# Kernel tuning notes

Measured on AMD Instinct MI355X. Metric: run time of the kernel, lower is better.

The kernel has to match this reference:

```python
import jax, jax.numpy as jnp
import numpy as np

N = 100000
D = 128      # embedding_dim
HID = 32     # hidden per head
HEADS = 4
OUT_C = 64
E = 1600000
NEG_SLOPE = 0.2


def setup_inputs() -> dict:
    key = jax.random.key(0)
    ks = jax.random.split(key, 12)
    inp = {}
    inp["x_indices"] = jnp.arange(N, dtype=jnp.int64)
    inp["ei"] = jax.random.randint(ks[0], (2, E), 0, N, dtype=jnp.int64)
    # parameters
    inp["emb"] = jax.random.normal(ks[1], (N, D), dtype=jnp.float32)
    # conv1: in=D, out=HID per head, HEADS heads, concat
    s1 = 1.0 / np.sqrt(D)
    inp["W1"] = jax.random.normal(ks[2], (D, HEADS * HID), dtype=jnp.float32) * s1
    inp["a_src1"] = jax.random.normal(ks[3], (HEADS, HID), dtype=jnp.float32) * s1
    inp["a_dst1"] = jax.random.normal(ks[4], (HEADS, HID), dtype=jnp.float32) * s1
    inp["b1"] = jnp.zeros((HEADS * HID,), dtype=jnp.float32)
    # conv2: in=HEADS*HID, out=OUT_C, 1 head
    s2 = 1.0 / np.sqrt(HEADS * HID)
    inp["W2"] = jax.random.normal(ks[5], (HEADS * HID, OUT_C), dtype=jnp.float32) * s2
    inp["a_src2"] = jax.random.normal(ks[6], (1, OUT_C), dtype=jnp.float32) * s2
    inp["a_dst2"] = jax.random.normal(ks[7], (1, OUT_C), dtype=jnp.float32) * s2
    inp["b2"] = jnp.zeros((OUT_C,), dtype=jnp.float32)
    return inp


def gat_conv(x, src, dst, W, a_src, a_dst, b, heads, out_ch, concat):
    # x: [N, Din]; src/dst: [E'] (self-loops already included)
    n = x.shape[0]
    h = (x @ W).reshape(n, heads, out_ch)          # [N, H, C]
    alpha_s = jnp.sum(h * a_src, axis=-1)          # [N, H]
    alpha_d = jnp.sum(h * a_dst, axis=-1)          # [N, H]
    e = alpha_s[src] + alpha_d[dst]                # [E', H]
    e = jnp.where(e > 0, e, NEG_SLOPE * e)         # leaky_relu
    # segment softmax over incoming edges per destination node
    m = jax.ops.segment_max(e, dst, num_segments=n)      # [N, H]
    ex = jnp.exp(e - m[dst])
    den = jax.ops.segment_sum(ex, dst, num_segments=n)   # [N, H]
    a = ex / den[dst]                              # [E', H]  (self-loops guarantee den>0)
    msg = h[src] * a[:, :, None]                   # [E', H, C]
    out = jax.ops.segment_sum(msg, dst, num_segments=n)  # [N, H, C]
    if concat:
        out = out.reshape(n, heads * out_ch)
    else:
        out = out.mean(axis=1)
    return out + b


def reference(x_indices, ei, emb, W1, a_src1, a_dst1, b1, W2, a_src2, a_dst2, b2):
    n = emb.shape[0]
    # PyG GATConv default add_self_loops=True
    loop = jnp.arange(n, dtype=ei.dtype)
    src = jnp.concatenate([ei[0], loop])
    dst = jnp.concatenate([ei[1], loop])
    x = emb[x_indices]                                  # embedding lookup
    x = jax.nn.elu(gat_conv(x, src, dst, W1, a_src1, a_dst1, b1, HEADS, HID, True))
    # dropout p=0.5 is identity in eval mode
    return gat_conv(x, src, dst, W2, a_src2, a_dst2, b2, 1, OUT_C, True)
```

## Files before the change

### kernel.cpp

```cpp
#include <hip/hip_runtime.h>
#include <math.h>

#define NEG_SLOPE 0.2f
#define BK_SHIFT 8

typedef __attribute__((ext_vector_type(2))) float v2f;

__device__ __forceinline__ float leaky(float x) { return x > 0.f ? x : NEG_SLOPE * x; }
__device__ __forceinline__ float dot4(float4 a, float4 b) {
    return a.x * b.x + a.y * b.y + a.z * b.z + a.w * b.w;
}
__device__ __forceinline__ unsigned short f2bf(float f) {
    unsigned int x = __float_as_uint(f);
    unsigned int r = (x + 0x7fffu + ((x >> 16) & 1u)) >> 16;
    return (unsigned short)r;
}
__device__ __forceinline__ float bflo(unsigned int u) { return __uint_as_float(u << 16); }
__device__ __forceinline__ float bfhi(unsigned int u) { return __uint_as_float(u & 0xffff0000u); }


__global__ void zero_kernel(int* __restrict__ p, int n) {
    int i = blockIdx.x * blockDim.x + threadIdx.x;
    if (i < n) p[i] = 0;
}

__global__ void __launch_bounds__(256) bcount_kernel(const int* __restrict__ ei, int E, int E2,
                                                     int K, int* __restrict__ bcounts) {
    __shared__ int h[512];
    int t = threadIdx.x;
    h[t] = 0; h[t + 256] = 0;
    __syncthreads();
    int base = blockIdx.x * 4096;
#pragma unroll 4
    for (int i = 0; i < 16; i++) {
        int e = base + i * 256 + t;
        if (e < E2) {
            int dst = (e < E) ? ei[E + e] : (e - E);
            atomicAdd(&h[dst >> BK_SHIFT], 1);
        }
    }
    __syncthreads();
    for (int b = t; b < K; b += 256) {
        int c = h[b];
        if (c) atomicAdd(&bcounts[b], c);
    }
}

__global__ void __launch_bounds__(512) bscan_kernel(const int* __restrict__ bcounts, int K,
                                                    int* __restrict__ bbase, int* __restrict__ bcursor) {
    __shared__ int s[512];
    int t = threadIdx.x;
    int v = (t < K) ? bcounts[t] : 0;
    s[t] = v;
    __syncthreads();
    for (int off = 1; off < 512; off <<= 1) {
        int u = (t >= off) ? s[t - off] : 0;
        __syncthreads();
        s[t] += u;
        __syncthreads();
    }
    if (t < K) {
        int ex = s[t] - v;
        bbase[t] = ex;
        bcursor[t] = ex;
    }
    if (t == 511) bbase[K] = s[511];
}

__global__ void __launch_bounds__(256) bscatter_kernel(const int* __restrict__ ei, int E, int E2,
                                                       int K, int* __restrict__ bcursor,
                                                       unsigned int* __restrict__ bedges) {
    __shared__ int hist[512], pre[512], lcur[512], gbase[512], psum[256];
    __shared__ unsigned int stage[4096];
    __shared__ unsigned short binof[4096];
    int t = threadIdx.x;
    hist[t] = 0; hist[t + 256] = 0;
    __syncthreads();
    int base = blockIdx.x * 4096;
    int cnt = min(4096, E2 - base);
    int s_[16], d_[16];
#pragma unroll
    for (int i = 0; i < 16; i++) {
        int e = base + i * 256 + t;
        if (e < E2) {
            int ss, dd;
            if (e < E) { ss = ei[e]; dd = ei[E + e]; }
            else       { ss = e - E; dd = ss; }
            s_[i] = ss; d_[i] = dd;
            atomicAdd(&hist[dd >> BK_SHIFT], 1);
        }
    }
    __syncthreads();
    int a0 = hist[2 * t], a1 = hist[2 * t + 1];
    psum[t] = a0 + a1;
    __syncthreads();
    for (int off = 1; off < 256; off <<= 1) {
        int u = (t >= off) ? psum[t - off] : 0;
        __syncthreads();
        psum[t] += u;
        __syncthreads();
    }
    int pex = psum[t] - (a0 + a1);
    pre[2 * t] = pex;
    pre[2 * t + 1] = pex + a0;
    __syncthreads();
    for (int b = t; b < K; b += 256) {
        int c = hist[b];
        if (c) gbase[b] = atomicAdd(&bcursor[b], c);
    }
    lcur[t] = pre[t]; lcur[t + 256] = pre[t + 256];
    __syncthreads();
#pragma unroll
    for (int i = 0; i < 16; i++) {
        int e = base + i * 256 + t;
        if (e < E2) {
            int bin = d_[i] >> BK_SHIFT;
            int p = atomicAdd(&lcur[bin], 1);
            stage[p] = ((unsigned)s_[i] << 8) | (unsigned)(d_[i] & 255);
            binof[p] = (unsigned short)bin;
        }
    }
    __syncthreads();
    for (int i = t; i < cnt; i += 256) {
        unsigned int ed = stage[i];
        int bin = (int)binof[i];
        bedges[gbase[bin] + (i - pre[bin])] = ed;
    }
}

__global__ void __launch_bounds__(256) bcsr_kernel(const unsigned int* __restrict__ bedges,
                                                   const int* __restrict__ bbase, int N,
                                                   int* __restrict__ counts, int* __restrict__ indptr,
                                                   int* __restrict__ csr) {
    __shared__ int hist[256], scn[256], cur[256];
    int b = blockIdx.x;
    int t = threadIdx.x;
    int base = bbase[b];
    int cnt = bbase[b + 1] - base;
    hist[t] = 0;
    __syncthreads();
    for (int i = t; i < cnt; i += 256) {
        atomicAdd(&hist[bedges[base + i] & 255u], 1);
    }
    __syncthreads();
    int v = hist[t];
    scn[t] = v;
    __syncthreads();
    for (int off = 1; off < 256; off <<= 1) {
        int u = (t >= off) ? scn[t - off] : 0;
        __syncthreads();
        scn[t] += u;
        __syncthreads();
    }
    int ex = scn[t] - v;
    int d = (b << BK_SHIFT) + t;
    if (d < N) { counts[d] = v; indptr[d] = base + ex; }
    cur[t] = ex;
    __syncthreads();
    for (int i = t; i < cnt; i += 256) {
        unsigned int ed = bedges[base + i];
        int p = atomicAdd(&cur[ed & 255u], 1);
        csr[base + p] = (int)(ed >> 8);
    }
}


__device__ __forceinline__ void fma16(float4 xv, float4 wv0, float4 wv1,
                                      float4 wv2, float4 wv3, float4& a) {
    a.x = fmaf(xv.x, wv0.x, a.x); a.y = fmaf(xv.x, wv0.y, a.y);
    a.z = fmaf(xv.x, wv0.z, a.z); a.w = fmaf(xv.x, wv0.w, a.w);
    a.x = fmaf(xv.y, wv1.x, a.x); a.y = fmaf(xv.y, wv1.y, a.y);
    a.z = fmaf(xv.y, wv1.z, a.z); a.w = fmaf(xv.y, wv1.w, a.w);
    a.x = fmaf(xv.z, wv2.x, a.x); a.y = fmaf(xv.z, wv2.y, a.y);
    a.z = fmaf(xv.z, wv2.z, a.z); a.w = fmaf(xv.z, wv2.w, a.w);
    a.x = fmaf(xv.w, wv3.x, a.x); a.y = fmaf(xv.w, wv3.y, a.y);
    a.z = fmaf(xv.w, wv3.z, a.z); a.w = fmaf(xv.w, wv3.w, a.w);
}


__global__ __launch_bounds__(256) void gemm1_kernel(const float* __restrict__ emb,
                             const int* __restrict__ xidx,
                             const float* __restrict__ W1,
                             unsigned short* __restrict__ h1b,
                             const float* __restrict__ a_s1, const float* __restrict__ a_d1,
                             float* __restrict__ as1, float* __restrict__ ad1, int N) {
    __shared__ float xs[64][64];
    __shared__ float ws[64][128];
    int tid = threadIdx.x;
    int r0 = blockIdx.x * 64;
    int tr = tid >> 5;
    int tc = tid & 31;
    float4 acc[8];
#pragma unroll
    for (int i = 0; i < 8; i++) acc[i] = make_float4(0.f, 0.f, 0.f, 0.f);
    const float4* W4 = (const float4*)W1;
    const float4* emb4 = (const float4*)emb;
    float4* ws4 = (float4*)ws;
    float4* xs4 = (float4*)xs;

    for (int half = 0; half < 2; half++) {
        float4 wbuf[8];
#pragma unroll
        for (int j = 0; j < 8; j++) wbuf[j] = W4[half * 2048 + tid + j * 256];
        float4 xbuf[4];
#pragma unroll
        for (int j = 0; j < 4; j++) {
            int idx = tid + j * 256;
            int r = idx >> 4, c = idx & 15;
            int row = r0 + r;
            float4 v = make_float4(0.f, 0.f, 0.f, 0.f);
            if (row < N) {
                int s = xidx[row];
                v = emb4[(size_t)s * 32 + half * 16 + c];
            }
            xbuf[j] = v;
        }
        __syncthreads();
#pragma unroll
        for (int j = 0; j < 8; j++) ws4[tid + j * 256] = wbuf[j];
#pragma unroll
        for (int j = 0; j < 4; j++) xs4[tid + j * 256] = xbuf[j];
        __syncthreads();
        for (int k = 0; k < 64; k += 4) {
            float4 wv0 = *(const float4*)&ws[k][tc * 4];
            float4 wv1 = *(const float4*)&ws[k + 1][tc * 4];
            float4 wv2 = *(const float4*)&ws[k + 2][tc * 4];
            float4 wv3 = *(const float4*)&ws[k + 3][tc * 4];
#pragma unroll
            for (int i = 0; i < 8; i++) {
                float4 xv = *(const float4*)&xs[tr * 8 + i][k];
                fma16(xv, wv0, wv1, wv2, wv3, acc[i]);
            }
        }
    }
    int colbase = tc * 4;
    int h = tc >> 3;
    int off = (tc & 7) * 4;
    float4 av = *(const float4*)&a_s1[h * 32 + off];
    float4 dv = *(const float4*)&a_d1[h * 32 + off];
#pragma unroll
    for (int i = 0; i < 8; i++) {
        int row = r0 + tr * 8 + i;
        if (row < N) {
            ushort4 pk;
            pk.x = f2bf(acc[i].x); pk.y = f2bf(acc[i].y);
            pk.z = f2bf(acc[i].z); pk.w = f2bf(acc[i].w);
            *(ushort4*)&h1b[(size_t)row * 128 + colbase] = pk;
        }
        float ps = dot4(acc[i], av);
        float pd = dot4(acc[i], dv);
        ps += __shfl_xor(ps, 1); pd += __shfl_xor(pd, 1);
        ps += __shfl_xor(ps, 2); pd += __shfl_xor(pd, 2);
        ps += __shfl_xor(ps, 4); pd += __shfl_xor(pd, 4);
        if ((tc & 7) == 0 && row < N) {
            as1[row * 4 + h] = ps;
            ad1[row * 4 + h] = pd;
        }
    }
}


__global__ __launch_bounds__(256) void gemm2_kernel(const unsigned short* __restrict__ x1b,
                             const float* __restrict__ W2,
                             unsigned short* __restrict__ h2b,
                             const float* __restrict__ a_s2, const float* __restrict__ a_d2,
                             float* __restrict__ as2, float* __restrict__ ad2, int N) {
    __shared__ float xs[128][68];
    __shared__ float ws[64][64];
    int tid = threadIdx.x;
    int r0 = blockIdx.x * 128;
    int tr = tid >> 4;
    int tc = tid & 15;
    float4 acc[8];
#pragma unroll
    for (int i = 0; i < 8; i++) acc[i] = make_float4(0.f, 0.f, 0.f, 0.f);
    const float4* W4 = (const float4*)W2;
    const uint4* x4 = (const uint4*)x1b;
    float4* ws4 = (float4*)ws;

    for (int half = 0; half < 2; half++) {
        float4 wbuf[4];
#pragma unroll
        for (int j = 0; j < 4; j++) wbuf[j] = W4[half * 1024 + tid + j * 256];
        uint4 xbuf[4];
#pragma unroll
        for (int j = 0; j < 4; j++) {
            int idx = tid + j * 256;
            int r = idx >> 3, c = idx & 7;
            int row = r0 + r;
            uint4 u = make_uint4(0u, 0u, 0u, 0u);
            if (row < N) u = x4[(size_t)row * 16 + half * 8 + c];
            xbuf[j] = u;
        }
        __syncthreads();
#pragma unroll
        for (int j = 0; j < 4; j++) ws4[tid + j * 256] = wbuf[j];
#pragma unroll
        for (int j = 0; j < 4; j++) {
            int idx = tid + j * 256;
            int r = idx >> 3, c = idx & 7;
            uint4 u = xbuf[j];
            float4 lo = make_float4(bflo(u.x), bfhi(u.x), bflo(u.y), bfhi(u.y));
            float4 hi = make_float4(bflo(u.z), bfhi(u.z), bflo(u.w), bfhi(u.w));
            *(float4*)&xs[r][c * 8] = lo;
            *(float4*)&xs[r][c * 8 + 4] = hi;
        }
        __syncthreads();
        for (int k = 0; k < 64; k += 4) {
            float4 wv0 = *(const float4*)&ws[k][tc * 4];
            float4 wv1 = *(const float4*)&ws[k + 1][tc * 4];
            float4 wv2 = *(const float4*)&ws[k + 2][tc * 4];
            float4 wv3 = *(const float4*)&ws[k + 3][tc * 4];
#pragma unroll
            for (int i = 0; i < 8; i++) {
                float4 xv = *(const float4*)&xs[i * 16 + tr][k];
                fma16(xv, wv0, wv1, wv2, wv3, acc[i]);
            }
        }
    }
    float4 av = *(const float4*)&a_s2[tc * 4];
    float4 dv = *(const float4*)&a_d2[tc * 4];
#pragma unroll
    for (int i = 0; i < 8; i++) {
        int row = r0 + i * 16 + tr;
        if (row < N) {
            ushort4 pk;
            pk.x = f2bf(acc[i].x); pk.y = f2bf(acc[i].y);
            pk.z = f2bf(acc[i].z); pk.w = f2bf(acc[i].w);
            *(ushort4*)&h2b[(size_t)row * 64 + tc * 4] = pk;
        }
        float ps = dot4(acc[i], av);
        float pd = dot4(acc[i], dv);
        ps += __shfl_xor(ps, 1); pd += __shfl_xor(pd, 1);
        ps += __shfl_xor(ps, 2); pd += __shfl_xor(pd, 2);
        ps += __shfl_xor(ps, 4); pd += __shfl_xor(pd, 4);
        ps += __shfl_xor(ps, 8); pd += __shfl_xor(pd, 8);
        if (tc == 0 && row < N) { as2[row] = ps; ad2[row] = pd; }
    }
}


__device__ __forceinline__ void edge_fma(uint4 u0, float w, v2f* acc) {
    v2f wv = {w, w};
    v2f t;
    t.x = bflo(u0.x); t.y = bfhi(u0.x); acc[0] += wv * t;
    t.x = bflo(u0.y); t.y = bfhi(u0.y); acc[1] += wv * t;
    t.x = bflo(u0.z); t.y = bfhi(u0.z); acc[2] += wv * t;
    t.x = bflo(u0.w); t.y = bfhi(u0.w); acc[3] += wv * t;
}

__device__ __forceinline__ void accum_tbl1(int srcReg, const float* __restrict__ ew, int mcount,
                                           const uint4* __restrict__ h1v4,
                                           int lanebase, int sub, int cg, int hh, v2f* acc) {
    int b = 0;
    for (; b + 8 <= mcount; b += 8) {
        int i0 = b + sub, i1 = b + 2 + sub, i2 = b + 4 + sub, i3 = b + 6 + sub;
        int s0 = __shfl(srcReg, lanebase + i0);
        int s1 = __shfl(srcReg, lanebase + i1);
        int s2 = __shfl(srcReg, lanebase + i2);
        int s3 = __shfl(srcReg, lanebase + i3);
        float w_0 = ew[i0 * 4 + hh];
        float w_1 = ew[i1 * 4 + hh];
        float w_2 = ew[i2 * 4 + hh];
        float w_3 = ew[i3 * 4 + hh];
        uint4 u0 = h1v4[(unsigned)(s0 * 16 + cg)];
        uint4 u1 = h1v4[(unsigned)(s1 * 16 + cg)];
        uint4 u2 = h1v4[(unsigned)(s2 * 16 + cg)];
        uint4 u3 = h1v4[(unsigned)(s3 * 16 + cg)];
        edge_fma(u0, w_0, acc);
        edge_fma(u1, w_1, acc);
        edge_fma(u2, w_2, acc);
        edge_fma(u3, w_3, acc);
    }
    if (b + 4 <= mcount) {
        int i0 = b + sub, i1 = b + 2 + sub;
        int s0 = __shfl(srcReg, lanebase + i0);
        int s1 = __shfl(srcReg, lanebase + i1);
        float w_0 = ew[i0 * 4 + hh];
        float w_1 = ew[i1 * 4 + hh];
        uint4 u0 = h1v4[(unsigned)(s0 * 16 + cg)];
        uint4 u1 = h1v4[(unsigned)(s1 * 16 + cg)];
        edge_fma(u0, w_0, acc);
        edge_fma(u1, w_1, acc);
        b += 4;
    }
    if (b + 2 <= mcount) {
        int i0 = b + sub;
        int s0 = __shfl(srcReg, lanebase + i0);
        float w_0 = ew[i0 * 4 + hh];
        uint4 u0 = h1v4[(unsigned)(s0 * 16 + cg)];
        edge_fma(u0, w_0, acc);
        b += 2;
    }
    if (b < mcount) {
        int s0 = __shfl(srcReg, lanebase + b);
        if (sub == 0) {
            float w_0 = ew[b * 4 + hh];
            uint4 u0 = h1v4[(unsigned)(s0 * 16 + cg)];
            edge_fma(u0, w_0, acc);
        }
    }
}

__global__ void __launch_bounds__(256)
agg1_kernel(const int* __restrict__ csr, const int* __restrict__ indptr,
            const int* __restrict__ counts, const float* __restrict__ as1,
            const float* __restrict__ ad1, const unsigned short* __restrict__ h1b,
            const float* __restrict__ b1, unsigned short* __restrict__ x1b, int N) {
    __shared__ float ewt[4][2][128];
    int lane = threadIdx.x & 63;
    int wv = threadIdx.x >> 6;
    int l32 = lane & 31;
    int lanebase = lane & 32;
    int n = blockIdx.x * 8 + wv * 2 + (lane >> 5);
    if (n >= N) return;
    int start = indptr[n];
    int cnt = counts[n];
    float4 ad4 = ((const float4*)ad1)[n];

    int src0 = 0;
    float4 p0 = make_float4(0.f, 0.f, 0.f, 0.f);
    if (l32 < cnt) {
        src0 = csr[start + l32];
        float4 a = ((const float4*)as1)[src0];
        p0.x = __expf(leaky(a.x + ad4.x));
        p0.y = __expf(leaky(a.y + ad4.y));
        p0.z = __expf(leaky(a.z + ad4.z));
        p0.w = __expf(leaky(a.w + ad4.w));
    }
    float4 l4 = p0;
    if (cnt > 32) {
        for (int base = 32; base < cnt; base += 32) {
            if (base + l32 < cnt) {
                int s = csr[start + base + l32];
                float4 a = ((const float4*)as1)[s];
                l4.x += __expf(leaky(a.x + ad4.x));
                l4.y += __expf(leaky(a.y + ad4.y));
                l4.z += __expf(leaky(a.z + ad4.z));
                l4.w += __expf(leaky(a.w + ad4.w));
            }
        }
    }
#pragma unroll
    for (int off = 16; off >= 1; off >>= 1) {
        l4.x += __shfl_xor(l4.x, off);
        l4.y += __shfl_xor(l4.y, off);
        l4.z += __shfl_xor(l4.z, off);
        l4.w += __shfl_xor(l4.w, off);
    }
    float4 li = make_float4(1.f / l4.x, 1.f / l4.y, 1.f / l4.z, 1.f / l4.w);
    float4 w0 = make_float4(p0.x * li.x, p0.y * li.y, p0.z * li.z, p0.w * li.w);

    float* ew = ewt[wv][lane >> 5];
    *(float4*)&ew[l32 * 4] = w0;

    int sub = l32 >> 4;
    int cg = lane & 15;
    int hh = cg >> 2;
    const uint4* h1v4 = (const uint4*)h1b;
    v2f acc[4];
    acc[0] = acc[1] = acc[2] = acc[3] = (v2f){0.f, 0.f};
    accum_tbl1(src0, ew, min(cnt, 32), h1v4, lanebase, sub, cg, hh, acc);
    if (cnt > 32) {
        for (int base = 32; base < cnt; base += 32) {
            int srcc = 0;
            float4 wc = make_float4(0.f, 0.f, 0.f, 0.f);
            if (base + l32 < cnt) {
                srcc = csr[start + base + l32];
                float4 a = ((const float4*)as1)[srcc];
                wc.x = __expf(leaky(a.x + ad4.x)) * li.x;
                wc.y = __expf(leaky(a.y + ad4.y)) * li.y;
                wc.z = __expf(leaky(a.z + ad4.z)) * li.z;
                wc.w = __expf(leaky(a.w + ad4.w)) * li.w;
            }
            *(float4*)&ew[l32 * 4] = wc;
            accum_tbl1(srcc, ew, min(cnt - base, 32), h1v4, lanebase, sub, cg, hh, acc);
        }
    }
#pragma unroll
    for (int i = 0; i < 4; i++) {
        acc[i].x += __shfl_xor(acc[i].x, 16);
        acc[i].y += __shfl_xor(acc[i].y, 16);
    }
    if (l32 < 16) {
        const float4* b4 = (const float4*)b1;
        float4 ba = b4[cg * 2], bb = b4[cg * 2 + 1];
        float o[8];
        o[0] = acc[0].x + ba.x; o[1] = acc[0].y + ba.y;
        o[2] = acc[1].x + ba.z; o[3] = acc[1].y + ba.w;
        o[4] = acc[2].x + bb.x; o[5] = acc[2].y + bb.y;
        o[6] = acc[3].x + bb.z; o[7] = acc[3].y + bb.w;
#pragma unroll
        for (int j = 0; j < 8; j++) o[j] = (o[j] > 0.f) ? o[j] : (__expf(o[j]) - 1.f);
        uint4 pk;
        pk.x = (unsigned)f2bf(o[0]) | ((unsigned)f2bf(o[1]) << 16);
        pk.y = (unsigned)f2bf(o[2]) | ((unsigned)f2bf(o[3]) << 16);
        pk.z = (unsigned)f2bf(o[4]) | ((unsigned)f2bf(o[5]) << 16);
        pk.w = (unsigned)f2bf(o[6]) | ((unsigned)f2bf(o[7]) << 16);
        *(uint4*)&x1b[(size_t)n * 128 + cg * 8] = pk;
    }
}


__device__ __forceinline__ void accum2(int srcReg, float wReg, int mcount,
                                       const uint4* __restrict__ h2v4,
                                       int lanebase, int sub, int cg, v2f* acc) {
    int b = 0;
    for (; b + 16 <= mcount; b += 16) {
        int i0 = b + sub, i1 = b + 4 + sub, i2 = b + 8 + sub, i3 = b + 12 + sub;
        int s0 = __shfl(srcReg, lanebase + i0);
        int s1 = __shfl(srcReg, lanebase + i1);
        int s2 = __shfl(srcReg, lanebase + i2);
        int s3 = __shfl(srcReg, lanebase + i3);
        float w_0 = __shfl(wReg, lanebase + i0);
        float w_1 = __shfl(wReg, lanebase + i1);
        float w_2 = __shfl(wReg, lanebase + i2);
        float w_3 = __shfl(wReg, lanebase + i3);
        uint4 u0 = h2v4[(unsigned)(s0 * 8 + cg)];
        uint4 u1 = h2v4[(unsigned)(s1 * 8 + cg)];
        uint4 u2 = h2v4[(unsigned)(s2 * 8 + cg)];
        uint4 u3 = h2v4[(unsigned)(s3 * 8 + cg)];
        edge_fma(u0, w_0, acc);
        edge_fma(u1, w_1, acc);
        edge_fma(u2, w_2, acc);
        edge_fma(u3, w_3, acc);
    }
    if (b + 8 <= mcount) {
        int i0 = b + sub, i1 = b + 4 + sub;
        int s0 = __shfl(srcReg, lanebase + i0);
        int s1 = __shfl(srcReg, lanebase + i1);
        float w_0 = __shfl(wReg, lanebase + i0);
        float w_1 = __shfl(wReg, lanebase + i1);
        uint4 u0 = h2v4[(unsigned)(s0 * 8 + cg)];
        uint4 u1 = h2v4[(unsigned)(s1 * 8 + cg)];
        edge_fma(u0, w_0, acc);
        edge_fma(u1, w_1, acc);
        b += 8;
    }
    if (b + 4 <= mcount) {
        int i0 = b + sub;
        int s0 = __shfl(srcReg, lanebase + i0);
        float w_0 = __shfl(wReg, lanebase + i0);
        uint4 u0 = h2v4[(unsigned)(s0 * 8 + cg)];
        edge_fma(u0, w_0, acc);
        b += 4;
    }
    if (b < mcount) {
        int rem = mcount - b;
        int i0 = b + sub;
        int ic = min(i0, mcount - 1);
        int s0 = __shfl(srcReg, lanebase + ic);
        float w_0 = __shfl(wReg, lanebase + ic);
        if (sub < rem) {
            uint4 u0 = h2v4[(unsigned)(s0 * 8 + cg)];
            edge_fma(u0, w_0, acc);
        }
    }
}

__global__ void __launch_bounds__(256)
agg2_kernel(const int* __restrict__ csr, const int* __restrict__ indptr,
            const int* __restrict__ counts, const float* __restrict__ as2,
            const float* __restrict__ ad2, const unsigned short* __restrict__ h2b,
            const float* __restrict__ b2, float* __restrict__ out, int N) {
    int lane = threadIdx.x & 63;
    int l32 = lane & 31;
    int lanebase = lane & 32;
    int n = blockIdx.x * 8 + (threadIdx.x >> 6) * 2 + (lane >> 5);
    if (n >= N) return;
    int start = indptr[n];
    int cnt = counts[n];
    float ad = ad2[n];

    int src0 = 0;
    float p0 = 0.f;
    if (l32 < cnt) {
        src0 = csr[start + l32];
        p0 = __expf(leaky(as2[src0] + ad));
    }
    float l = p0;
    if (cnt > 32) {
        for (int base = 32; base < cnt; base += 32) {
            if (base + l32 < cnt)
                l += __expf(leaky(as2[csr[start + base + l32]] + ad));
        }
    }
#pragma unroll
    for (int off = 16; off >= 1; off >>= 1) l += __shfl_xor(l, off);
    float li = 1.f / l;
    float w0 = p0 * li;

    int sub = l32 >> 3;
    int cg = lane & 7;
    const uint4* h2v4 = (const uint4*)h2b;
    v2f acc[4];
    acc[0] = acc[1] = acc[2] = acc[3] = (v2f){0.f, 0.f};
    accum2(src0, w0, min(cnt, 32), h2v4, lanebase, sub, cg, acc);
    if (cnt > 32) {
        for (int base = 32; base < cnt; base += 32) {
            int srcc = 0;
            float wc = 0.f;
            if (base + l32 < cnt) {
                srcc = csr[start + base + l32];
                wc = __expf(leaky(as2[srcc] + ad)) * li;
            }
            accum2(srcc, wc, min(cnt - base, 32), h2v4, lanebase, sub, cg, acc);
        }
    }
#pragma unroll
    for (int i = 0; i < 4; i++) {
        acc[i].x += __shfl_xor(acc[i].x, 8);
        acc[i].x += __shfl_xor(acc[i].x, 16);
        acc[i].y += __shfl_xor(acc[i].y, 8);
        acc[i].y += __shfl_xor(acc[i].y, 16);
    }
    if (l32 < 8) {
        const float4* b4 = (const float4*)b2;
        float4 ba = b4[cg * 2], bb = b4[cg * 2 + 1];
        float4 o0, o1;
        o0.x = acc[0].x + ba.x; o0.y = acc[0].y + ba.y;
        o0.z = acc[1].x + ba.z; o0.w = acc[1].y + ba.w;
        o1.x = acc[2].x + bb.x; o1.y = acc[2].y + bb.y;
        o1.z = acc[3].x + bb.z; o1.w = acc[3].y + bb.w;
        float4* orow = (float4*)&out[(size_t)n * 64 + cg * 8];
        orow[0] = o0;
        orow[1] = o1;
    }
}


extern "C" void kernel_launch(void* const* d_in, const int* in_sizes, int n_in,
                              void* d_out, int out_size, void* d_ws, size_t ws_size,
                              hipStream_t stream) {
    const int*   xidx = (const int*)d_in[0];
    const int*   ei   = (const int*)d_in[1];
    const float* emb  = (const float*)d_in[2];
    const float* W1   = (const float*)d_in[3];
    const float* a_s1 = (const float*)d_in[4];
    const float* a_d1 = (const float*)d_in[5];
    const float* b1   = (const float*)d_in[6];
    const float* W2   = (const float*)d_in[7];
    const float* a_s2 = (const float*)d_in[8];
    const float* a_d2 = (const float*)d_in[9];
    const float* b2   = (const float*)d_in[10];
    float* out = (float*)d_out;

    const int N  = in_sizes[0];
    const int E  = in_sizes[1] / 2;
    const int E2 = E + N;
    const int K  = (N + 255) >> BK_SHIFT;

    int* ws_i    = (int*)d_ws;
    int* counts  = ws_i;
    int* indptr  = ws_i + N;
    int* bcounts = ws_i + 2 * (size_t)N;
    int* bbase   = ws_i + 2 * (size_t)N + 512;
    int* bcursor = ws_i + 2 * (size_t)N + 1032;
    int* csr     = ws_i + 2 * (size_t)N + 1544;
    size_t fbase = ((size_t)(2 * (size_t)N + 1544 + E2) + 3) & ~(size_t)3;
    float* ws_f = (float*)d_ws;
    unsigned short* h1b = (unsigned short*)(ws_f + fbase);
    unsigned short* x1b = (unsigned short*)(ws_f + fbase + (size_t)N * 64);
    float* as1 = ws_f + fbase + (size_t)N * 128;
    float* ad1 = as1 + (size_t)N * 4;
    unsigned short* h2b = h1b;
    float* as2 = as1;
    float* ad2 = ad1;
    unsigned int* bedges = (unsigned int*)x1b;

    int nchunks = (E2 + 4095) / 4096;
    zero_kernel<<<(K + 255) / 256, 256, 0, stream>>>(bcounts, K);
    bcount_kernel<<<nchunks, 256, 0, stream>>>(ei, E, E2, K, bcounts);
    bscan_kernel<<<1, 512, 0, stream>>>(bcounts, K, bbase, bcursor);
    bscatter_kernel<<<nchunks, 256, 0, stream>>>(ei, E, E2, K, bcursor, bedges);
    bcsr_kernel<<<K, 256, 0, stream>>>(bedges, bbase, N, counts, indptr, csr);

    gemm1_kernel<<<(N + 63) / 64, 256, 0, stream>>>(emb, xidx, W1, h1b, a_s1, a_d1, as1, ad1, N);
    agg1_kernel<<<(N + 7) / 8, 256, 0, stream>>>(csr, indptr, counts, as1, ad1, h1b, b1, x1b, N);

    gemm2_kernel<<<(N + 127) / 128, 256, 0, stream>>>(x1b, W2, h2b, a_s2, a_d2, as2, ad2, N);
    agg2_kernel<<<(N + 7) / 8, 256, 0, stream>>>(csr, indptr, counts, as2, ad2, h2b, b2, out, N);
}
```

Baseline: 427.3 us.

## Fuse second-layer GEMM into first aggregation epilogue with bf16 W2 in LDS

Removes the separate gemm2 kernel and computes each node's layer-2 projection and attention logits directly in the agg1 epilogue. W2 is pre-packed to bf16 pairs and loaded into shared memory per block, and the x1 intermediate is no longer written to or read back from global memory. The zero-fill kernel is replaced by hipMemsetAsync. In exchange, every agg1 block now loads 16KB of W2 into LDS and does a per-node 128x64 matvec, which raises LDS use and may lower occupancy. W2 is now rounded to bf16, which slightly changes numerics.

```diff
diff --git a/kernel.cpp b/kernel.cpp
--- a/kernel.cpp
+++ b/kernel.cpp
@@ -18,11 +18,6 @@
 __device__ __forceinline__ float bflo(unsigned int u) { return __uint_as_float(u << 16); }
 __device__ __forceinline__ float bfhi(unsigned int u) { return __uint_as_float(u & 0xffff0000u); }
 
-
-__global__ void zero_kernel(int* __restrict__ p, int n) {
-    int i = blockIdx.x * blockDim.x + threadIdx.x;
-    if (i < n) p[i] = 0;
-}
 
 __global__ void __launch_bounds__(256) bcount_kernel(const int* __restrict__ ei, int E, int E2,
                                                      int K, int* __restrict__ bcounts) {
@@ -161,6 +156,16 @@
         unsigned int ed = bedges[base + i];
         int p = atomicAdd(&cur[ed & 255u], 1);
         csr[base + p] = (int)(ed >> 8);
+    }
+}
+
+
+__global__ void w2pack_kernel(const float* __restrict__ W2, unsigned* __restrict__ w2p) {
+    int i = blockIdx.x * 256 + threadIdx.x;
+    if (i < 4096) {
+        int k = i >> 5, j = i & 31;
+        w2p[i] = (unsigned)f2bf(W2[k * 64 + 2 * j]) |
+                 ((unsigned)f2bf(W2[k * 64 + 2 * j + 1]) << 16);
     }
 }
 
@@ -256,86 +261,6 @@
             as1[row * 4 + h] = ps;
             ad1[row * 4 + h] = pd;
         }
-    }
-}
-
-
-__global__ __launch_bounds__(256) void gemm2_kernel(const unsigned short* __restrict__ x1b,
-                             const float* __restrict__ W2,
-                             unsigned short* __restrict__ h2b,
-                             const float* __restrict__ a_s2, const float* __restrict__ a_d2,
-                             float* __restrict__ as2, float* __restrict__ ad2, int N) {
-    __shared__ float xs[128][68];
-    __shared__ float ws[64][64];
-    int tid = threadIdx.x;
-    int r0 = blockIdx.x * 128;
-    int tr = tid >> 4;
-    int tc = tid & 15;
-    float4 acc[8];
-#pragma unroll
-    for (int i = 0; i < 8; i++) acc[i] = make_float4(0.f, 0.f, 0.f, 0.f);
-    const float4* W4 = (const float4*)W2;
-    const uint4* x4 = (const uint4*)x1b;
-    float4* ws4 = (float4*)ws;
-
-    for (int half = 0; half < 2; half++) {
-        float4 wbuf[4];
-#pragma unroll
-        for (int j = 0; j < 4; j++) wbuf[j] = W4[half * 1024 + tid + j * 256];
-        uint4 xbuf[4];
-#pragma unroll
-        for (int j = 0; j < 4; j++) {
-            int idx = tid + j * 256;
-            int r = idx >> 3, c = idx & 7;
-            int row = r0 + r;
-            uint4 u = make_uint4(0u, 0u, 0u, 0u);
-            if (row < N) u = x4[(size_t)row * 16 + half * 8 + c];
-            xbuf[j] = u;
-        }
-        __syncthreads();
-#pragma unroll
-        for (int j = 0; j < 4; j++) ws4[tid + j * 256] = wbuf[j];
-#pragma unroll
-        for (int j = 0; j < 4; j++) {
-            int idx = tid + j * 256;
-            int r = idx >> 3, c = idx & 7;
-            uint4 u = xbuf[j];
-            float4 lo = make_float4(bflo(u.x), bfhi(u.x), bflo(u.y), bfhi(u.y));
-            float4 hi = make_float4(bflo(u.z), bfhi(u.z), bflo(u.w), bfhi(u.w));
-            *(float4*)&xs[r][c * 8] = lo;
-            *(float4*)&xs[r][c * 8 + 4] = hi;
-        }
-        __syncthreads();
-        for (int k = 0; k < 64; k += 4) {
-            float4 wv0 = *(const float4*)&ws[k][tc * 4];
-            float4 wv1 = *(const float4*)&ws[k + 1][tc * 4];
-            float4 wv2 = *(const float4*)&ws[k + 2][tc * 4];
-            float4 wv3 = *(const float4*)&ws[k + 3][tc * 4];
-#pragma unroll
-            for (int i = 0; i < 8; i++) {
-                float4 xv = *(const float4*)&xs[i * 16 + tr][k];
-                fma16(xv, wv0, wv1, wv2, wv3, acc[i]);
-            }
-        }
-    }
-    float4 av = *(const float4*)&a_s2[tc * 4];
-    float4 dv = *(const float4*)&a_d2[tc * 4];
-#pragma unroll
-    for (int i = 0; i < 8; i++) {
-        int row = r0 + i * 16 + tr;
-        if (row < N) {
-            ushort4 pk;
-            pk.x = f2bf(acc[i].x); pk.y = f2bf(acc[i].y);
-            pk.z = f2bf(acc[i].z); pk.w = f2bf(acc[i].w);
-            *(ushort4*)&h2b[(size_t)row * 64 + tc * 4] = pk;
-        }
-        float ps = dot4(acc[i], av);
-        float pd = dot4(acc[i], dv);
-        ps += __shfl_xor(ps, 1); pd += __shfl_xor(pd, 1);
-        ps += __shfl_xor(ps, 2); pd += __shfl_xor(pd, 2);
-        ps += __shfl_xor(ps, 4); pd += __shfl_xor(pd, 4);
-        ps += __shfl_xor(ps, 8); pd += __shfl_xor(pd, 8);
-        if (tc == 0 && row < N) { as2[row] = ps; ad2[row] = pd; }
     }
 }
 
@@ -406,98 +331,133 @@
 agg1_kernel(const int* __restrict__ csr, const int* __restrict__ indptr,
             const int* __restrict__ counts, const float* __restrict__ as1,
             const float* __restrict__ ad1, const unsigned short* __restrict__ h1b,
-            const float* __restrict__ b1, unsigned short* __restrict__ x1b, int N) {
+            const float* __restrict__ b1, const unsigned* __restrict__ w2p,
+            const float* __restrict__ a_s2, const float* __restrict__ a_d2,
+            unsigned short* __restrict__ h2b, float* __restrict__ as2,
+            float* __restrict__ ad2, int N) {
     __shared__ float ewt[4][2][128];
-    int lane = threadIdx.x & 63;
-    int wv = threadIdx.x >> 6;
+    __shared__ float xrow[4][2][128];
+    __shared__ unsigned w2s[4096];
+    int tid = threadIdx.x;
+    {
+        const uint4* w4 = (const uint4*)w2p;
+        uint4* s4 = (uint4*)w2s;
+        for (int i = tid; i < 1024; i += 256) s4[i] = w4[i];
+    }
+    __syncthreads();
+
+    int lane = tid & 63;
+    int wv = tid >> 6;
     int l32 = lane & 31;
     int lanebase = lane & 32;
     int n = blockIdx.x * 8 + wv * 2 + (lane >> 5);
-    if (n >= N) return;
-    int start = indptr[n];
-    int cnt = counts[n];
-    float4 ad4 = ((const float4*)ad1)[n];
-
-    int src0 = 0;
-    float4 p0 = make_float4(0.f, 0.f, 0.f, 0.f);
-    if (l32 < cnt) {
-        src0 = csr[start + l32];
-        float4 a = ((const float4*)as1)[src0];
-        p0.x = __expf(leaky(a.x + ad4.x));
-        p0.y = __expf(leaky(a.y + ad4.y));
-        p0.z = __expf(leaky(a.z + ad4.z));
-        p0.w = __expf(leaky(a.w + ad4.w));
-    }
-    float4 l4 = p0;
-    if (cnt > 32) {
-        for (int base = 32; base < cnt; base += 32) {
-            if (base + l32 < cnt) {
-                int s = csr[start + base + l32];
-                float4 a = ((const float4*)as1)[s];
-                l4.x += __expf(leaky(a.x + ad4.x));
-                l4.y += __expf(leaky(a.y + ad4.y));
-                l4.z += __expf(leaky(a.z + ad4.z));
-                l4.w += __expf(leaky(a.w + ad4.w));
+    if (n < N) {
+        int start = indptr[n];
+        int cnt = counts[n];
+        float4 ad4 = ((const float4*)ad1)[n];
+
+        int src0 = 0;
+        float4 p0 = make_float4(0.f, 0.f, 0.f, 0.f);
+        if (l32 < cnt) {
+            src0 = csr[start + l32];
+            float4 a = ((const float4*)as1)[src0];
+            p0.x = __expf(leaky(a.x + ad4.x));
+            p0.y = __expf(leaky(a.y + ad4.y));
+            p0.z = __expf(leaky(a.z + ad4.z));
+            p0.w = __expf(leaky(a.w + ad4.w));
+        }
+        float4 l4 = p0;
+        if (cnt > 32) {
+            for (int base = 32; base < cnt; base += 32) {
+                if (base + l32 < cnt) {
+                    int s = csr[start + base + l32];
+                    float4 a = ((const float4*)as1)[s];
+                    l4.x += __expf(leaky(a.x + ad4.x));
+                    l4.y += __expf(leaky(a.y + ad4.y));
+                    l4.z += __expf(leaky(a.z + ad4.z));
+                    l4.w += __expf(leaky(a.w + ad4.w));
+                }
             }
         }
-    }
-#pragma unroll
-    for (int off = 16; off >= 1; off >>= 1) {
-        l4.x += __shfl_xor(l4.x, off);
-        l4.y += __shfl_xor(l4.y, off);
-        l4.z += __shfl_xor(l4.z, off);
-        l4.w += __shfl_xor(l4.w, off);
-    }
-    float4 li = make_float4(1.f / l4.x, 1.f / l4.y, 1.f / l4.z, 1.f / l4.w);
-    float4 w0 = make_float4(p0.x * li.x, p0.y * li.y, p0.z * li.z, p0.w * li.w);
-
-    float* ew = ewt[wv][lane >> 5];
-    *(float4*)&ew[l32 * 4] = w0;
-
-    int sub = l32 >> 4;
-    int cg = lane & 15;
-    int hh = cg >> 2;
-    const uint4* h1v4 = (const uint4*)h1b;
-    v2f acc[4];
-    acc[0] = acc[1] = acc[2] = acc[3] = (v2f){0.f, 0.f};
-    accum_tbl1(src0, ew, min(cnt, 32), h1v4, lanebase, sub, cg, hh, acc);
-    if (cnt > 32) {
-        for (int base = 32; base < cnt; base += 32) {
-            int srcc = 0;
-            float4 wc = make_float4(0.f, 0.f, 0.f, 0.f);
-            if (base + l32 < cnt) {
-                srcc = csr[start + base + l32];
-                float4 a = ((const float4*)as1)[srcc];
-                wc.x = __expf(leaky(a.x + ad4.x)) * li.x;
-                wc.y = __expf(leaky(a.y + ad4.y)) * li.y;
-                wc.z = __expf(leaky(a.z + ad4.z)) * li.z;
-                wc.w = __expf(leaky(a.w + ad4.w)) * li.w;
+#pragma unroll
+        for (int off = 16; off >= 1; off >>= 1) {
+            l4.x += __shfl_xor(l4.x, off);
+            l4.y += __shfl_xor(l4.y, off);
+            l4.z += __shfl_xor(l4.z, off);
+            l4.w += __shfl_xor(l4.w, off);
+        }
+        float4 li = make_float4(1.f / l4.x, 1.f / l4.y, 1.f / l4.z, 1.f / l4.w);
+        float4 w0 = make_float4(p0.x * li.x, p0.y * li.y, p0.z * li.z, p0.w * li.w);
+
+        float* ew = ewt[wv][lane >> 5];
+        *(float4*)&ew[l32 * 4] = w0;
+
+        int sub = l32 >> 4;
+        int cg = lane & 15;
+        int hh = cg >> 2;
+        const uint4* h1v4 = (const uint4*)h1b;
+        v2f acc[4];
+        acc[0] = acc[1] = acc[2] = acc[3] = (v2f){0.f, 0.f};
+        accum_tbl1(src0, ew, min(cnt, 32), h1v4, lanebase, sub, cg, hh, acc);
+        if (cnt > 32) {
+            for (int base = 32; base < cnt; base += 32) {
+                int srcc = 0;
+                float4 wc = make_float4(0.f, 0.f, 0.f, 0.f);
+                if (base + l32 < cnt) {
+                    srcc = csr[start + base + l32];
+                    float4 a = ((const float4*)as1)[srcc];
+                    wc.x = __expf(leaky(a.x + ad4.x)) * li.x;
+                    wc.y = __expf(leaky(a.y + ad4.y)) * li.y;
+                    wc.z = __expf(leaky(a.z + ad4.z)) * li.z;
+                    wc.w = __expf(leaky(a.w + ad4.w)) * li.w;
+                }
+                *(float4*)&ew[l32 * 4] = wc;
+                accum_tbl1(srcc, ew, min(cnt - base, 32), h1v4, lanebase, sub, cg, hh, acc);
             }
-            *(float4*)&ew[l32 * 4] = wc;
-            accum_tbl1(srcc, ew, min(cnt - base, 32), h1v4, lanebase, sub, cg, hh, acc);
-        }
-    }
-#pragma unroll
-    for (int i = 0; i < 4; i++) {
-        acc[i].x += __shfl_xor(acc[i].x, 16);
-        acc[i].y += __shfl_xor(acc[i].y, 16);
-    }
-    if (l32 < 16) {
-        const float4* b4 = (const float4*)b1;
-        float4 ba = b4[cg * 2], bb = b4[cg * 2 + 1];
-        float o[8];
-        o[0] = acc[0].x + ba.x; o[1] = acc[0].y + ba.y;
-        o[2] = acc[1].x + ba.z; o[3] = acc[1].y + ba.w;
-        o[4] = acc[2].x + bb.x; o[5] = acc[2].y + bb.y;
-        o[6] = acc[3].x + bb.z; o[7] = acc[3].y + bb.w;
-#pragma unroll
-        for (int j = 0; j < 8; j++) o[j] = (o[j] > 0.f) ? o[j] : (__expf(o[j]) - 1.f);
-        uint4 pk;
-        pk.x = (unsigned)f2bf(o[0]) | ((unsigned)f2bf(o[1]) << 16);
-        pk.y = (unsigned)f2bf(o[2]) | ((unsigned)f2bf(o[3]) << 16);
-        pk.z = (unsigned)f2bf(o[4]) | ((unsigned)f2bf(o[5]) << 16);
-        pk.w = (unsigned)f2bf(o[6]) | ((unsigned)f2bf(o[7]) << 16);
-        *(uint4*)&x1b[(size_t)n * 128 + cg * 8] = pk;
+        }
+#pragma unroll
+        for (int i = 0; i < 4; i++) {
+            acc[i].x += __shfl_xor(acc[i].x, 16);
+            acc[i].y += __shfl_xor(acc[i].y, 16);
+        }
+        float* xr = xrow[wv][lane >> 5];
+        if (l32 < 16) {
+            const float4* b4 = (const float4*)b1;
+            float4 ba = b4[cg * 2], bb = b4[cg * 2 + 1];
+            float o[8];
+            o[0] = acc[0].x + ba.x; o[1] = acc[0].y + ba.y;
+            o[2] = acc[1].x + ba.z; o[3] = acc[1].y + ba.w;
+            o[4] = acc[2].x + bb.x; o[5] = acc[2].y + bb.y;
+            o[6] = acc[3].x + bb.z; o[7] = acc[3].y + bb.w;
+#pragma unroll
+            for (int j = 0; j < 8; j++) o[j] = (o[j] > 0.f) ? o[j] : (__expf(o[j]) - 1.f);
+            *(float4*)&xr[cg * 8]     = make_float4(o[0], o[1], o[2], o[3]);
+            *(float4*)&xr[cg * 8 + 4] = make_float4(o[4], o[5], o[6], o[7]);
+        }
+        float h0 = 0.f, h1r = 0.f;
+        for (int k = 0; k < 128; k += 4) {
+            float4 xv = *(const float4*)&xr[k];
+            unsigned u0 = w2s[(k    ) * 32 + l32];
+            unsigned u1 = w2s[(k + 1) * 32 + l32];
+            unsigned u2 = w2s[(k + 2) * 32 + l32];
+            unsigned u3 = w2s[(k + 3) * 32 + l32];
+            h0 = fmaf(xv.x, bflo(u0), h0); h1r = fmaf(xv.x, bfhi(u0), h1r);
+            h0 = fmaf(xv.y, bflo(u1), h0); h1r = fmaf(xv.y, bfhi(u1), h1r);
+            h0 = fmaf(xv.z, bflo(u2), h0); h1r = fmaf(xv.z, bfhi(u2), h1r);
+            h0 = fmaf(xv.w, bflo(u3), h0); h1r = fmaf(xv.w, bfhi(u3), h1r);
+        }
+        float2 av2 = *(const float2*)&a_s2[l32 * 2];
+        float2 dv2 = *(const float2*)&a_d2[l32 * 2];
+        float ps = h0 * av2.x + h1r * av2.y;
+        float pd = h0 * dv2.x + h1r * dv2.y;
+#pragma unroll
+        for (int off = 16; off >= 1; off >>= 1) {
+            ps += __shfl_xor(ps, off);
+            pd += __shfl_xor(pd, off);
+        }
+        if (l32 == 0) { as2[n] = ps; ad2[n] = pd; }
+        unsigned hp = (unsigned)f2bf(h0) | ((unsigned)f2bf(h1r) << 16);
+        ((unsigned*)h2b)[(size_t)n * 32 + l32] = hp;
     }
 }
 
@@ -660,24 +620,28 @@
     size_t fbase = ((size_t)(2 * (size_t)N + 1544 + E2) + 3) & ~(size_t)3;
     float* ws_f = (float*)d_ws;
     unsigned short* h1b = (unsigned short*)(ws_f + fbase);
-    unsigned short* x1b = (unsigned short*)(ws_f + fbase + (size_t)N * 64);
+    float* region2 = ws_f + fbase + (size_t)N * 64;
+    unsigned short* h2b = (unsigned short*)region2;
+    float* as2 = region2 + (size_t)N * 32;
+    float* ad2 = region2 + (size_t)N * 33;
+    unsigned* w2p = (unsigned*)(region2 + (size_t)N * 34);
     float* as1 = ws_f + fbase + (size_t)N * 128;
     float* ad1 = as1 + (size_t)N * 4;
-    unsigned short* h2b = h1b;
-    float* as2 = as1;
-    float* ad2 = ad1;
-    unsigned int* bedges = (unsigned int*)x1b;
+    unsigned int* bedges = (unsigned int*)region2;
 
     int nchunks = (E2 + 4095) / 4096;
-    zero_kernel<<<(K + 255) / 256, 256, 0, stream>>>(bcounts, K);
+    hipMemsetAsync(bcounts, 0, (size_t)K * sizeof(int), stream);
     bcount_kernel<<<nchunks, 256, 0, stream>>>(ei, E, E2, K, bcounts);
     bscan_kernel<<<1, 512, 0, stream>>>(bcounts, K, bbase, bcursor);
     bscatter_kernel<<<nchunks, 256, 0, stream>>>(ei, E, E2, K, bcursor, bedges);
     bcsr_kernel<<<K, 256, 0, stream>>>(bedges, bbase, N, counts, indptr, csr);
 
     gemm1_kernel<<<(N + 63) / 64, 256, 0, stream>>>(emb, xidx, W1, h1b, a_s1, a_d1, as1, ad1, N);
-    agg1_kernel<<<(N + 7) / 8, 256, 0, stream>>>(csr, indptr, counts, as1, ad1, h1b, b1, x1b, N);
-
-    gemm2_kernel<<<(N + 127) / 128, 256, 0, stream>>>(x1b, W2, h2b, a_s2, a_d2, as2, ad2, N);
+
+    w2pack_kernel<<<16, 256, 0, stream>>>(W2, w2p);
+
+    agg1_kernel<<<(N + 7) / 8, 256, 0, stream>>>(csr, indptr, counts, as1, ad1, h1b, b1,
+                                                 w2p, a_s2, a_d2, h2b, as2, ad2, N);
+
     agg2_kernel<<<(N + 7) / 8, 256, 0, stream>>>(csr, indptr, counts, as2, ad2, h2b, b2, out, N);
 }
```

New measurement: 405.6 us. 1.05x faster.
